# Kernel optimization log

Hardware: AMD Instinct MI355X
Metric: run time of the kernel (lower is better)

The kernel has to match this reference:

```python
import jax, jax.numpy as jnp
import numpy as np

B, N, C_IN, D, K = 4, 512, 256, 256, 20


def setup_inputs() -> dict:
    key = jax.random.key(0)
    ks = jax.random.split(key, 6)
    s_in = 1.0 / np.sqrt(C_IN)
    return {
        "x": jax.random.normal(ks[0], (B, N, C_IN), dtype=jnp.float32),
        "edge_index": jnp.zeros((2, 4), dtype=jnp.int64),
        "batch": jnp.zeros((B * N,), dtype=jnp.int64),
        "W_l": jax.random.uniform(ks[1], (D, C_IN), jnp.float32, -s_in, s_in),
        "b_l": jax.random.uniform(ks[2], (D,), jnp.float32, -s_in, s_in),
        "W_r": jax.random.uniform(ks[3], (D, C_IN), jnp.float32, -s_in, s_in),
        "b_r": jax.random.uniform(ks[4], (D,), jnp.float32, -s_in, s_in),
        "att": jax.random.normal(ks[5], (1, D), dtype=jnp.float32) * 0.1,
    }


def reference(x, edge_index, batch, W_l, b_l, W_r, b_r, att):
    b, n, _ = x.shape
    k = K
    # linear projections -> [b, n, d]
    x_l = jnp.einsum("bnc,dc->bnd", x, W_l) + b_l
    x_r = jnp.einsum("bnc,dc->bnd", x, W_r) + b_r
    # pairwise additive attention: [b, n, n, d]
    pair = x_l[:, :, None, :] + x_r[:, None, :, :]
    pair = jnp.where(pair >= 0, pair, 0.2 * pair)  # leaky_relu(0.2)
    alpha = jnp.einsum("bijd,d->bij", pair, att[0])  # [b, n, n]
    alpha = jnp.nan_to_num(alpha, nan=0.0, posinf=0.0, neginf=0.0)
    # knn reduction: topk over last dim
    attention, indices = jax.lax.top_k(alpha, k)  # [b, n, k]
    attention = jax.nn.softmax(attention, axis=-1).reshape(-1)  # [b*n*k]
    # edge index construction with per-batch node offsets
    offset = (jnp.arange(b, dtype=indices.dtype) * n)[:, None]  # [b, 1]
    index_i = jnp.repeat(jnp.arange(n, dtype=indices.dtype), k)[None, :] + offset
    index_j = indices.reshape(b, n * k) + offset
    new_edge_index = jnp.stack([index_i.reshape(-1), index_j.reshape(-1)], axis=0)
    # dropout is identity in eval mode; learn_sys=False -> return directly
    return new_edge_index, attention
```

## Files before the change

### kernel.cpp

```cpp
#include <hip/hip_runtime.h>
#include <math.h>


__global__ __launch_bounds__(256) void k_transpose(const float* __restrict__ Wl,
                                                   const float* __restrict__ Wr,
                                                   float* __restrict__ WtL,
                                                   float* __restrict__ WtR) {
    const int d = blockIdx.x, c = threadIdx.x;
    if (blockIdx.y == 0) WtL[c * 256 + d] = Wl[d * 256 + c];
    else                 WtR[c * 256 + d] = Wr[d * 256 + c];
}

__global__ __launch_bounds__(256) void k_proj(const float* __restrict__ x,
        const float* __restrict__ WtL, const float* __restrict__ WtR,
        const float* __restrict__ bl, const float* __restrict__ br,
        const float* __restrict__ att,
        float* __restrict__ XL, float* __restrict__ XRt,
        float* __restrict__ Av, float* __restrict__ Bv) {
    __shared__ float xs[4 * 256];
    __shared__ float red[32];
    const int tid = threadIdx.x;
    const int R = blockIdx.x * 4;

    ((float4*)xs)[tid] = ((const float4*)(x + (size_t)R * 256))[tid];
    __syncthreads();

    float accL[4] = {0.f, 0.f, 0.f, 0.f}, accR[4] = {0.f, 0.f, 0.f, 0.f};
    for (int c = 0; c < 256; c += 4) {
        const float wl0 = WtL[(c + 0) * 256 + tid];
        const float wl1 = WtL[(c + 1) * 256 + tid];
        const float wl2 = WtL[(c + 2) * 256 + tid];
        const float wl3 = WtL[(c + 3) * 256 + tid];
        const float wr0 = WtR[(c + 0) * 256 + tid];
        const float wr1 = WtR[(c + 1) * 256 + tid];
        const float wr2 = WtR[(c + 2) * 256 + tid];
        const float wr3 = WtR[(c + 3) * 256 + tid];
#pragma unroll
        for (int r = 0; r < 4; ++r) {
            const float4 xv = *(const float4*)&xs[r * 256 + c];
            accL[r] = fmaf(xv.x, wl0, accL[r]);
            accL[r] = fmaf(xv.y, wl1, accL[r]);
            accL[r] = fmaf(xv.z, wl2, accL[r]);
            accL[r] = fmaf(xv.w, wl3, accL[r]);
            accR[r] = fmaf(xv.x, wr0, accR[r]);
            accR[r] = fmaf(xv.y, wr1, accR[r]);
            accR[r] = fmaf(xv.z, wr2, accR[r]);
            accR[r] = fmaf(xv.w, wr3, accR[r]);
        }
    }

    const float blv = bl[tid], brv = br[tid], atv = att[tid];
    float xlv[4], xrv[4], pa[4], pb[4];
#pragma unroll
    for (int r = 0; r < 4; ++r) {
        xlv[r] = accL[r] + blv;
        xrv[r] = accR[r] + brv;
        XL[(size_t)(R + r) * 256 + tid] = xlv[r];
        pa[r] = atv * xlv[r];
        pb[r] = atv * xrv[r];
    }
    const int b = R >> 9, jr = R & 511;
    *(float4*)&XRt[((size_t)(b * 256 + tid)) * 512 + jr] =
        make_float4(xrv[0], xrv[1], xrv[2], xrv[3]);

#pragma unroll
    for (int r = 0; r < 4; ++r) {
#pragma unroll
        for (int off = 32; off; off >>= 1) {
            pa[r] += __shfl_xor(pa[r], off);
            pb[r] += __shfl_xor(pb[r], off);
        }
    }
    const int lane = tid & 63, wv = tid >> 6;
    if (lane == 0) {
#pragma unroll
        for (int r = 0; r < 4; ++r) {
            red[r * 8 + wv] = pa[r];
            red[r * 8 + 4 + wv] = pb[r];
        }
    }
    __syncthreads();
    if (tid < 8) {
        const int r = tid >> 1, side = tid & 1;
        const float* p = &red[r * 8 + side * 4];
        const float s = p[0] + p[1] + p[2] + p[3];
        if (side == 0) Av[R + r] = s; else Bv[R + r] = s;
    }
}

__global__ __launch_bounds__(256) void k_pair(const float* __restrict__ XL,
        const float* __restrict__ XRt, const float* __restrict__ Av,
        const float* __restrict__ Bv, const float* __restrict__ att,
        float* __restrict__ alpha) {
    const int tid = threadIdx.x;
    const int g = blockIdx.x;
    const int jh = g & 1;
    const int ig = g >> 1;
    const int b = ig >> 6;
    const int R = b * 512 + (ig & 63) * 8;
    const int j = jh * 256 + tid;

    const float* __restrict__ XLr = XL + (size_t)R * 256;
    const float* __restrict__ xrp = XRt + ((size_t)b * 256) * 512 + j;

    float acc[8];
#pragma unroll
    for (int i = 0; i < 8; ++i) acc[i] = 0.f;

    for (int d = 0; d < 256; d += 8) {
        float xr[8];
#pragma unroll
        for (int dd = 0; dd < 8; ++dd) xr[dd] = xrp[dd * 512];
#pragma unroll
        for (int dd = 0; dd < 8; ++dd) {
            const float a = att[d + dd];
#pragma unroll
            for (int i = 0; i < 8; ++i) {
                const float v = XLr[i * 256 + d + dd] + xr[dd];
                acc[i] = fmaf(a, fabsf(v), acc[i]);
            }
        }
        xrp += 8 * 512;
    }

    const float Bj = Bv[b * 512 + j];
#pragma unroll
    for (int i = 0; i < 8; ++i) {
        float a = fmaf(0.4f, acc[i], 0.6f * (Av[R + i] + Bj));
        if (!isfinite(a)) a = 0.f;
        alpha[(size_t)(R + i) * 512 + j] = a;
    }
}

__global__ __launch_bounds__(256) void k_topk(const float* __restrict__ alpha,
                                              float* __restrict__ out) {
    const int lane = threadIdx.x & 63;
    const int row = blockIdx.x * 4 + (threadIdx.x >> 6);
    const float* ar = alpha + (size_t)row * 512;

    const float4 u0 = *(const float4*)&ar[lane * 8];
    const float4 u1 = *(const float4*)&ar[lane * 8 + 4];
    float v[8] = {u0.x, u0.y, u0.z, u0.w, u1.x, u1.y, u1.z, u1.w};

    float myval = 0.f, mmax = 0.f;
    int myidx = 0;
    for (int sel = 0; sel < 20; ++sel) {
        float bv = v[0]; int bt = 0;
#pragma unroll
        for (int t = 1; t < 8; ++t) { if (v[t] > bv) { bv = v[t]; bt = t; } }
        int bj = lane * 8 + bt;
#pragma unroll
        for (int off = 32; off; off >>= 1) {
            const float ov = __shfl_xor(bv, off);
            const int   oj = __shfl_xor(bj, off);
            if (ov > bv || (ov == bv && oj < bj)) { bv = ov; bj = oj; }
        }
        if (sel == 0) mmax = bv;
        if (lane == sel) { myval = bv; myidx = bj; }
        if ((bj >> 3) == lane) {
            const int bt2 = bj & 7;
#pragma unroll
            for (int t = 0; t < 8; ++t) if (t == bt2) v[t] = -INFINITY;
        }
    }
    const float e = (lane < 20) ? expf(myval - mmax) : 0.f;
    float s = e;
#pragma unroll
    for (int off = 32; off; off >>= 1) s += __shfl_xor(s, off);
    if (lane < 20) {
        const int base = row * 20 + lane;
        const int b = row >> 9;
        out[base] = (float)row;
        out[40960 + base] = (float)(b * 512 + myidx);
        out[81920 + base] = e / s;
    }
}

extern "C" void kernel_launch(void* const* d_in, const int* in_sizes, int n_in,
                              void* d_out, int out_size, void* d_ws, size_t ws_size,
                              hipStream_t stream) {
    const float* x   = (const float*)d_in[0];
    const float* Wl  = (const float*)d_in[3];
    const float* bl  = (const float*)d_in[4];
    const float* Wr  = (const float*)d_in[5];
    const float* br  = (const float*)d_in[6];
    const float* att = (const float*)d_in[7];

    float* ws    = (float*)d_ws;
    float* WtL   = ws;
    float* WtR   = ws + 65536;
    float* alpha = ws;
    float* XL    = ws + 1048576;
    float* XRt   = ws + 1572864;
    float* Av    = ws + 2097152;
    float* Bv    = ws + 2099200;
    float* out   = (float*)d_out;

    k_transpose<<<dim3(256, 2), dim3(256), 0, stream>>>(Wl, Wr, WtL, WtR);
    k_proj<<<dim3(512), dim3(256), 0, stream>>>(x, WtL, WtR, bl, br, att, XL, XRt, Av, Bv);
    k_pair<<<dim3(512), dim3(256), 0, stream>>>(XL, XRt, Av, Bv, att, alpha);
    k_topk<<<dim3(512), dim3(256), 0, stream>>>(alpha, out);
}
```

Measured before the change: 138.7 us.

## Split pair kernel reduction over two d-halves with register prefetch

The pairwise attention kernel now launches twice as many blocks, each covering 128 columns, and splits the 256-long feature reduction between two halves of the block. The halves are merged through shared memory. XRt loads are double-buffered in registers to overlap with compute, and the att and XL loads are vectorized as float4. This aims to add parallelism and hide memory latency, at the cost of a sync, shared-memory traffic, and idle threads during the final write.

```diff
diff --git a/kernel.cpp b/kernel.cpp
--- a/kernel.cpp
+++ b/kernel.cpp
@@ -92,43 +92,73 @@
         const float* __restrict__ XRt, const float* __restrict__ Av,
         const float* __restrict__ Bv, const float* __restrict__ att,
         float* __restrict__ alpha) {
+    __shared__ float mrg[128 * 8];
     const int tid = threadIdx.x;
     const int g = blockIdx.x;
-    const int jh = g & 1;
-    const int ig = g >> 1;
-    const int b = ig >> 6;
-    const int R = b * 512 + (ig & 63) * 8;
-    const int j = jh * 256 + tid;
+    const int jq = g & 3;
+    const int io = g >> 2;
+    const int b = io >> 6;
+    const int R = b * 512 + (io & 63) * 8;
+    const int jl = tid & 127;
+    const int h = tid >> 7;
+    const int j = jq * 128 + jl;
+    const int dbase = h * 128;
 
     const float* __restrict__ XLr = XL + (size_t)R * 256;
-    const float* __restrict__ xrp = XRt + ((size_t)b * 256) * 512 + j;
+    const float* __restrict__ xrp = XRt + ((size_t)(b * 256 + dbase)) * 512 + j;
 
     float acc[8];
 #pragma unroll
     for (int i = 0; i < 8; ++i) acc[i] = 0.f;
 
-    for (int d = 0; d < 256; d += 8) {
-        float xr[8];
-#pragma unroll
-        for (int dd = 0; dd < 8; ++dd) xr[dd] = xrp[dd * 512];
-#pragma unroll
-        for (int dd = 0; dd < 8; ++dd) {
-            const float a = att[d + dd];
-#pragma unroll
-            for (int i = 0; i < 8; ++i) {
-                const float v = XLr[i * 256 + d + dd] + xr[dd];
-                acc[i] = fmaf(a, fabsf(v), acc[i]);
-            }
-        }
-        xrp += 8 * 512;
-    }
-
-    const float Bj = Bv[b * 512 + j];
-#pragma unroll
-    for (int i = 0; i < 8; ++i) {
-        float a = fmaf(0.4f, acc[i], 0.6f * (Av[R + i] + Bj));
-        if (!isfinite(a)) a = 0.f;
-        alpha[(size_t)(R + i) * 512 + j] = a;
+    float xrbuf[2][8];
+#pragma unroll
+    for (int dd = 0; dd < 8; ++dd) xrbuf[0][dd] = xrp[dd * 512];
+
+#pragma unroll
+    for (int ch = 0; ch < 16; ++ch) {
+        const float* cur = xrbuf[ch & 1];
+        float* nxt = xrbuf[(ch + 1) & 1];
+        if (ch < 15) {
+            const float* p = xrp + (size_t)(ch + 1) * 8 * 512;
+#pragma unroll
+            for (int dd = 0; dd < 8; ++dd) nxt[dd] = p[dd * 512];
+        }
+        const int d = dbase + ch * 8;
+        const float4 at0 = *(const float4*)&att[d];
+        const float4 at1 = *(const float4*)&att[d + 4];
+#pragma unroll
+        for (int i = 0; i < 8; ++i) {
+            const float4 xa = *(const float4*)&XLr[i * 256 + d];
+            const float4 xb = *(const float4*)&XLr[i * 256 + d + 4];
+            acc[i] = fmaf(at0.x, fabsf(xa.x + cur[0]), acc[i]);
+            acc[i] = fmaf(at0.y, fabsf(xa.y + cur[1]), acc[i]);
+            acc[i] = fmaf(at0.z, fabsf(xa.z + cur[2]), acc[i]);
+            acc[i] = fmaf(at0.w, fabsf(xa.w + cur[3]), acc[i]);
+            acc[i] = fmaf(at1.x, fabsf(xb.x + cur[4]), acc[i]);
+            acc[i] = fmaf(at1.y, fabsf(xb.y + cur[5]), acc[i]);
+            acc[i] = fmaf(at1.z, fabsf(xb.z + cur[6]), acc[i]);
+            acc[i] = fmaf(at1.w, fabsf(xb.w + cur[7]), acc[i]);
+        }
+    }
+
+    if (h == 1) {
+        *(float4*)&mrg[jl * 8 + 0] = make_float4(acc[0], acc[1], acc[2], acc[3]);
+        *(float4*)&mrg[jl * 8 + 4] = make_float4(acc[4], acc[5], acc[6], acc[7]);
+    }
+    __syncthreads();
+    if (h == 0) {
+        const float4 m0 = *(const float4*)&mrg[jl * 8 + 0];
+        const float4 m1 = *(const float4*)&mrg[jl * 8 + 4];
+        acc[0] += m0.x; acc[1] += m0.y; acc[2] += m0.z; acc[3] += m0.w;
+        acc[4] += m1.x; acc[5] += m1.y; acc[6] += m1.z; acc[7] += m1.w;
+        const float Bj = Bv[b * 512 + j];
+#pragma unroll
+        for (int i = 0; i < 8; ++i) {
+            float a = fmaf(0.4f, acc[i], 0.6f * (Av[R + i] + Bj));
+            if (!isfinite(a)) a = 0.f;
+            alpha[(size_t)(R + i) * 512 + j] = a;
+        }
     }
 }
 
@@ -198,6 +228,6 @@
 
     k_transpose<<<dim3(256, 2), dim3(256), 0, stream>>>(Wl, Wr, WtL, WtR);
     k_proj<<<dim3(512), dim3(256), 0, stream>>>(x, WtL, WtR, bl, br, att, XL, XRt, Av, Bv);
-    k_pair<<<dim3(512), dim3(256), 0, stream>>>(XL, XRt, Av, Bv, att, alpha);
+    k_pair<<<dim3(1024), dim3(256), 0, stream>>>(XL, XRt, Av, Bv, att, alpha);
     k_topk<<<dim3(512), dim3(256), 0, stream>>>(alpha, out);
 }
```

Measured after the change: 144.1 us. 1.04x slower.

## Fuse pairwise attention and top-k into one kernel with split-d reduction

Applied to the files above, without the earlier changes.

Merges the pairwise alpha kernel and the top-k kernel so the 4x512 alpha rows stay in shared memory instead of making a round trip through global memory. Each block now handles 4 query rows over all 512 columns, splitting the d dimension across two thread halves and merging the partial sums through LDS. XRt is loaded as float4 with register double-buffering. The change cuts global traffic and one launch, but each block does less row reuse (4 rows instead of 8) and uses more shared memory, which may lower occupancy.

```diff
diff --git a/kernel.cpp b/kernel.cpp
--- a/kernel.cpp
+++ b/kernel.cpp
@@ -88,56 +88,100 @@
     }
 }
 
-__global__ __launch_bounds__(256) void k_pair(const float* __restrict__ XL,
+__global__ __launch_bounds__(256) void k_pair_topk(const float* __restrict__ XL,
         const float* __restrict__ XRt, const float* __restrict__ Av,
         const float* __restrict__ Bv, const float* __restrict__ att,
-        float* __restrict__ alpha) {
+        float* __restrict__ out) {
+    __shared__ float xls[4 * 256];
+    __shared__ float atts[256];
+    __shared__ float mrg[16 * 128];
+    __shared__ float alph[4 * 512];
     const int tid = threadIdx.x;
     const int g = blockIdx.x;
-    const int jh = g & 1;
-    const int ig = g >> 1;
-    const int b = ig >> 6;
-    const int R = b * 512 + (ig & 63) * 8;
-    const int j = jh * 256 + tid;
-
-    const float* __restrict__ XLr = XL + (size_t)R * 256;
-    const float* __restrict__ xrp = XRt + ((size_t)b * 256) * 512 + j;
-
-    float acc[8];
-#pragma unroll
-    for (int i = 0; i < 8; ++i) acc[i] = 0.f;
-
-    for (int d = 0; d < 256; d += 8) {
-        float xr[8];
-#pragma unroll
-        for (int dd = 0; dd < 8; ++dd) xr[dd] = xrp[dd * 512];
-#pragma unroll
-        for (int dd = 0; dd < 8; ++dd) {
-            const float a = att[d + dd];
-#pragma unroll
-            for (int i = 0; i < 8; ++i) {
-                const float v = XLr[i * 256 + d + dd] + xr[dd];
-                acc[i] = fmaf(a, fabsf(v), acc[i]);
-            }
-        }
-        xrp += 8 * 512;
-    }
-
-    const float Bj = Bv[b * 512 + j];
-#pragma unroll
-    for (int i = 0; i < 8; ++i) {
-        float a = fmaf(0.4f, acc[i], 0.6f * (Av[R + i] + Bj));
-        if (!isfinite(a)) a = 0.f;
-        alpha[(size_t)(R + i) * 512 + j] = a;
-    }
-}
-
-__global__ __launch_bounds__(256) void k_topk(const float* __restrict__ alpha,
-                                              float* __restrict__ out) {
-    const int lane = threadIdx.x & 63;
-    const int row = blockIdx.x * 4 + (threadIdx.x >> 6);
-    const float* ar = alpha + (size_t)row * 512;
-
+    const int R = g * 4;
+    const int b = R >> 9;
+    const int jc = tid & 127;
+    const int h = tid >> 7;
+
+    ((float4*)xls)[tid] = ((const float4*)(XL + (size_t)R * 256))[tid];
+    if (tid < 64) ((float4*)atts)[tid] = ((const float4*)att)[tid];
+    __syncthreads();
+
+    const float* xrbase = XRt + ((size_t)(b * 256 + h * 128)) * 512 + jc * 4;
+    const int dbase = h * 128;
+
+    float4 acc[4];
+#pragma unroll
+    for (int i = 0; i < 4; ++i) acc[i] = make_float4(0.f, 0.f, 0.f, 0.f);
+
+    float4 buf[2][8];
+#pragma unroll
+    for (int dd = 0; dd < 8; ++dd) buf[0][dd] = *(const float4*)(xrbase + dd * 512);
+
+#pragma unroll
+    for (int ch = 0; ch < 16; ++ch) {
+        const float4* cur = buf[ch & 1];
+        float4* nxt = buf[(ch + 1) & 1];
+        if (ch < 15) {
+            const float* p = xrbase + (size_t)(ch + 1) * 8 * 512;
+#pragma unroll
+            for (int dd = 0; dd < 8; ++dd) nxt[dd] = *(const float4*)(p + dd * 512);
+        }
+        const int d = dbase + ch * 8;
+        const float4 at0 = *(const float4*)&atts[d];
+        const float4 at1 = *(const float4*)&atts[d + 4];
+#pragma unroll
+        for (int i = 0; i < 4; ++i) {
+            const float4 xa = *(const float4*)&xls[i * 256 + d];
+            const float4 xb = *(const float4*)&xls[i * 256 + d + 4];
+#define PSTEP(XLC, ATC, XR4)                                   \
+            acc[i].x = fmaf(ATC, fabsf(XLC + XR4.x), acc[i].x); \
+            acc[i].y = fmaf(ATC, fabsf(XLC + XR4.y), acc[i].y); \
+            acc[i].z = fmaf(ATC, fabsf(XLC + XR4.z), acc[i].z); \
+            acc[i].w = fmaf(ATC, fabsf(XLC + XR4.w), acc[i].w);
+            PSTEP(xa.x, at0.x, cur[0])
+            PSTEP(xa.y, at0.y, cur[1])
+            PSTEP(xa.z, at0.z, cur[2])
+            PSTEP(xa.w, at0.w, cur[3])
+            PSTEP(xb.x, at1.x, cur[4])
+            PSTEP(xb.y, at1.y, cur[5])
+            PSTEP(xb.z, at1.z, cur[6])
+            PSTEP(xb.w, at1.w, cur[7])
+#undef PSTEP
+        }
+    }
+
+    if (h == 1) {
+#pragma unroll
+        for (int i = 0; i < 4; ++i) {
+            mrg[(i * 4 + 0) * 128 + jc] = acc[i].x;
+            mrg[(i * 4 + 1) * 128 + jc] = acc[i].y;
+            mrg[(i * 4 + 2) * 128 + jc] = acc[i].z;
+            mrg[(i * 4 + 3) * 128 + jc] = acc[i].w;
+        }
+    }
+    __syncthreads();
+    if (h == 0) {
+        const float4 Bj = *(const float4*)&Bv[b * 512 + jc * 4];
+#pragma unroll
+        for (int i = 0; i < 4; ++i) {
+            const float Ai = Av[R + i];
+            float a0 = fmaf(0.4f, acc[i].x + mrg[(i * 4 + 0) * 128 + jc], 0.6f * (Ai + Bj.x));
+            float a1 = fmaf(0.4f, acc[i].y + mrg[(i * 4 + 1) * 128 + jc], 0.6f * (Ai + Bj.y));
+            float a2 = fmaf(0.4f, acc[i].z + mrg[(i * 4 + 2) * 128 + jc], 0.6f * (Ai + Bj.z));
+            float a3 = fmaf(0.4f, acc[i].w + mrg[(i * 4 + 3) * 128 + jc], 0.6f * (Ai + Bj.w));
+            if (!isfinite(a0)) a0 = 0.f;
+            if (!isfinite(a1)) a1 = 0.f;
+            if (!isfinite(a2)) a2 = 0.f;
+            if (!isfinite(a3)) a3 = 0.f;
+            *(float4*)&alph[i * 512 + jc * 4] = make_float4(a0, a1, a2, a3);
+        }
+    }
+    __syncthreads();
+
+    const int lane = tid & 63;
+    const int i = tid >> 6;
+    const float* ar = &alph[i * 512];
     const float4 u0 = *(const float4*)&ar[lane * 8];
     const float4 u1 = *(const float4*)&ar[lane * 8 + 4];
     float v[8] = {u0.x, u0.y, u0.z, u0.w, u1.x, u1.y, u1.z, u1.w};
@@ -168,8 +212,8 @@
 #pragma unroll
     for (int off = 32; off; off >>= 1) s += __shfl_xor(s, off);
     if (lane < 20) {
+        const int row = R + i;
         const int base = row * 20 + lane;
-        const int b = row >> 9;
         out[base] = (float)row;
         out[40960 + base] = (float)(b * 512 + myidx);
         out[81920 + base] = e / s;
@@ -189,7 +233,6 @@
     float* ws    = (float*)d_ws;
     float* WtL   = ws;
     float* WtR   = ws + 65536;
-    float* alpha = ws;
     float* XL    = ws + 1048576;
     float* XRt   = ws + 1572864;
     float* Av    = ws + 2097152;
@@ -198,6 +241,5 @@
 
     k_transpose<<<dim3(256, 2), dim3(256), 0, stream>>>(Wl, Wr, WtL, WtR);
     k_proj<<<dim3(512), dim3(256), 0, stream>>>(x, WtL, WtR, bl, br, att, XL, XRt, Av, Bv);
-    k_pair<<<dim3(512), dim3(256), 0, stream>>>(XL, XRt, Av, Bv, att, alpha);
-    k_topk<<<dim3(512), dim3(256), 0, stream>>>(alpha, out);
-}
+    k_pair_topk<<<dim3(512), dim3(256), 0, stream>>>(XL, XRt, Av, Bv, att, out);
+}
```

After: 122.4 us. 11.8% less time.

## Fuse pairwise attention with top-k and retile projection with split-K reduction

Applied to the files above, without the earlier changes.

The pairwise-score kernel and the top-k kernel are merged, so each block computes alpha for 4 rows into shared memory and runs the top-k/softmax there, removing the global alpha round-trip. XRt slices are streamed into a double-buffered LDS staging area with direct global-to-LDS loads. The projection kernel is retiled to 8 rows per 512-thread block with a 4-way split over the input channel and an LDS merge, using float4 weight loads. In exchange, the fused kernel has only 512 blocks of 128 threads and a large LDS footprint, which may limit occupancy.

```diff
diff --git a/kernel.cpp b/kernel.cpp
--- a/kernel.cpp
+++ b/kernel.cpp
@@ -1,6 +1,11 @@
 #include <hip/hip_runtime.h>
 #include <math.h>
 
+
+#define GLD_LDS(gp, lp)                                                        \
+    __builtin_amdgcn_global_load_lds(                                          \
+        (const __attribute__((address_space(1))) float*)(gp),                  \
+        (__attribute__((address_space(3))) float*)(lp), 16, 0, 0)
 
 __global__ __launch_bounds__(256) void k_transpose(const float* __restrict__ Wl,
                                                    const float* __restrict__ Wr,
@@ -11,168 +16,256 @@
     else                 WtR[c * 256 + d] = Wr[d * 256 + c];
 }
 
-__global__ __launch_bounds__(256) void k_proj(const float* __restrict__ x,
+__global__ __launch_bounds__(512, 4) void k_proj(const float* __restrict__ x,
         const float* __restrict__ WtL, const float* __restrict__ WtR,
         const float* __restrict__ bl, const float* __restrict__ br,
         const float* __restrict__ att,
         float* __restrict__ XL, float* __restrict__ XRt,
         float* __restrict__ Av, float* __restrict__ Bv) {
-    __shared__ float xs[4 * 256];
-    __shared__ float red[32];
+    __shared__ __align__(16) float xst[256 * 12];
+    __shared__ __align__(16) float mrg[3 * 4096];
     const int tid = threadIdx.x;
-    const int R = blockIdx.x * 4;
-
-    ((float4*)xs)[tid] = ((const float4*)(x + (size_t)R * 256))[tid];
+    const int dq = tid & 63;
+    const int rq = (tid >> 6) & 1;
+    const int ch = tid >> 7;
+    const int R = blockIdx.x * 8;
+    const int b = R >> 9, jr0 = R & 511;
+
+    {
+        const float4 xv = ((const float4*)(x + (size_t)R * 256))[tid];
+        const int r = tid >> 6;
+        const int c4 = (tid & 63) * 4;
+        xst[(c4 + 0) * 12 + r] = xv.x;
+        xst[(c4 + 1) * 12 + r] = xv.y;
+        xst[(c4 + 2) * 12 + r] = xv.z;
+        xst[(c4 + 3) * 12 + r] = xv.w;
+    }
     __syncthreads();
 
-    float accL[4] = {0.f, 0.f, 0.f, 0.f}, accR[4] = {0.f, 0.f, 0.f, 0.f};
-    for (int c = 0; c < 256; c += 4) {
-        const float wl0 = WtL[(c + 0) * 256 + tid];
-        const float wl1 = WtL[(c + 1) * 256 + tid];
-        const float wl2 = WtL[(c + 2) * 256 + tid];
-        const float wl3 = WtL[(c + 3) * 256 + tid];
-        const float wr0 = WtR[(c + 0) * 256 + tid];
-        const float wr1 = WtR[(c + 1) * 256 + tid];
-        const float wr2 = WtR[(c + 2) * 256 + tid];
-        const float wr3 = WtR[(c + 3) * 256 + tid];
+    float aL[4][4], aR[4][4];
+#pragma unroll
+    for (int r = 0; r < 4; ++r)
+#pragma unroll
+        for (int k = 0; k < 4; ++k) { aL[r][k] = 0.f; aR[r][k] = 0.f; }
+
+    const int c0 = ch * 64;
+    const float* WLp = WtL + (size_t)c0 * 256 + dq * 4;
+    const float* WRp = WtR + (size_t)c0 * 256 + dq * 4;
+#pragma unroll 4
+    for (int cc = 0; cc < 64; ++cc) {
+        const float4 wl = *(const float4*)(WLp + (size_t)cc * 256);
+        const float4 wr = *(const float4*)(WRp + (size_t)cc * 256);
+        const float4 xv = *(const float4*)&xst[(c0 + cc) * 12 + rq * 4];
+#define PROJ_R(r, XS)                                  \
+        aL[r][0] = fmaf(XS, wl.x, aL[r][0]);           \
+        aL[r][1] = fmaf(XS, wl.y, aL[r][1]);           \
+        aL[r][2] = fmaf(XS, wl.z, aL[r][2]);           \
+        aL[r][3] = fmaf(XS, wl.w, aL[r][3]);           \
+        aR[r][0] = fmaf(XS, wr.x, aR[r][0]);           \
+        aR[r][1] = fmaf(XS, wr.y, aR[r][1]);           \
+        aR[r][2] = fmaf(XS, wr.z, aR[r][2]);           \
+        aR[r][3] = fmaf(XS, wr.w, aR[r][3]);
+        PROJ_R(0, xv.x)
+        PROJ_R(1, xv.y)
+        PROJ_R(2, xv.z)
+        PROJ_R(3, xv.w)
+#undef PROJ_R
+    }
+
+    if (ch > 0) {
+        float* m = &mrg[(ch - 1) * 4096];
 #pragma unroll
         for (int r = 0; r < 4; ++r) {
-            const float4 xv = *(const float4*)&xs[r * 256 + c];
-            accL[r] = fmaf(xv.x, wl0, accL[r]);
-            accL[r] = fmaf(xv.y, wl1, accL[r]);
-            accL[r] = fmaf(xv.z, wl2, accL[r]);
-            accL[r] = fmaf(xv.w, wl3, accL[r]);
-            accR[r] = fmaf(xv.x, wr0, accR[r]);
-            accR[r] = fmaf(xv.y, wr1, accR[r]);
-            accR[r] = fmaf(xv.z, wr2, accR[r]);
-            accR[r] = fmaf(xv.w, wr3, accR[r]);
-        }
-    }
-
-    const float blv = bl[tid], brv = br[tid], atv = att[tid];
-    float xlv[4], xrv[4], pa[4], pb[4];
-#pragma unroll
-    for (int r = 0; r < 4; ++r) {
-        xlv[r] = accL[r] + blv;
-        xrv[r] = accR[r] + brv;
-        XL[(size_t)(R + r) * 256 + tid] = xlv[r];
-        pa[r] = atv * xlv[r];
-        pb[r] = atv * xrv[r];
-    }
-    const int b = R >> 9, jr = R & 511;
-    *(float4*)&XRt[((size_t)(b * 256 + tid)) * 512 + jr] =
-        make_float4(xrv[0], xrv[1], xrv[2], xrv[3]);
-
-#pragma unroll
-    for (int r = 0; r < 4; ++r) {
-#pragma unroll
-        for (int off = 32; off; off >>= 1) {
-            pa[r] += __shfl_xor(pa[r], off);
-            pb[r] += __shfl_xor(pb[r], off);
-        }
-    }
-    const int lane = tid & 63, wv = tid >> 6;
-    if (lane == 0) {
+            const int r8 = rq * 4 + r;
+            *(float4*)&m[(r8 * 2 + 0) * 256 + dq * 4] = make_float4(aL[r][0], aL[r][1], aL[r][2], aL[r][3]);
+            *(float4*)&m[(r8 * 2 + 1) * 256 + dq * 4] = make_float4(aR[r][0], aR[r][1], aR[r][2], aR[r][3]);
+        }
+    }
+    __syncthreads();
+
+    if (ch == 0) {
+        const float4 bl4 = *(const float4*)&bl[dq * 4];
+        const float4 br4 = *(const float4*)&br[dq * 4];
+        const float4 at4 = *(const float4*)&att[dq * 4];
+        float pa[4], pb[4];
 #pragma unroll
         for (int r = 0; r < 4; ++r) {
-            red[r * 8 + wv] = pa[r];
-            red[r * 8 + 4 + wv] = pb[r];
-        }
-    }
-    __syncthreads();
-    if (tid < 8) {
-        const int r = tid >> 1, side = tid & 1;
-        const float* p = &red[r * 8 + side * 4];
-        const float s = p[0] + p[1] + p[2] + p[3];
-        if (side == 0) Av[R + r] = s; else Bv[R + r] = s;
-    }
-}
-
-__global__ __launch_bounds__(256) void k_pair(const float* __restrict__ XL,
+            const int r8 = rq * 4 + r;
+            const float4 mL0 = *(const float4*)&mrg[(r8 * 2 + 0) * 256 + dq * 4];
+            const float4 mL1 = *(const float4*)&mrg[4096 + (r8 * 2 + 0) * 256 + dq * 4];
+            const float4 mL2 = *(const float4*)&mrg[8192 + (r8 * 2 + 0) * 256 + dq * 4];
+            const float4 mR0 = *(const float4*)&mrg[(r8 * 2 + 1) * 256 + dq * 4];
+            const float4 mR1 = *(const float4*)&mrg[4096 + (r8 * 2 + 1) * 256 + dq * 4];
+            const float4 mR2 = *(const float4*)&mrg[8192 + (r8 * 2 + 1) * 256 + dq * 4];
+            float4 sl, sr;
+            sl.x = aL[r][0] + mL0.x + mL1.x + mL2.x + bl4.x;
+            sl.y = aL[r][1] + mL0.y + mL1.y + mL2.y + bl4.y;
+            sl.z = aL[r][2] + mL0.z + mL1.z + mL2.z + bl4.z;
+            sl.w = aL[r][3] + mL0.w + mL1.w + mL2.w + bl4.w;
+            sr.x = aR[r][0] + mR0.x + mR1.x + mR2.x + br4.x;
+            sr.y = aR[r][1] + mR0.y + mR1.y + mR2.y + br4.y;
+            sr.z = aR[r][2] + mR0.z + mR1.z + mR2.z + br4.z;
+            sr.w = aR[r][3] + mR0.w + mR1.w + mR2.w + br4.w;
+            *(float4*)&XL[(size_t)(R + r8) * 256 + dq * 4] = sl;
+            const size_t xrb0 = ((size_t)(b * 256 + dq * 4)) * 512 + jr0 + r8;
+            XRt[xrb0 + 0 * 512] = sr.x;
+            XRt[xrb0 + 1 * 512] = sr.y;
+            XRt[xrb0 + 2 * 512] = sr.z;
+            XRt[xrb0 + 3 * 512] = sr.w;
+            pa[r] = at4.x * sl.x + at4.y * sl.y + at4.z * sl.z + at4.w * sl.w;
+            pb[r] = at4.x * sr.x + at4.y * sr.y + at4.z * sr.z + at4.w * sr.w;
+        }
+#pragma unroll
+        for (int r = 0; r < 4; ++r) {
+#pragma unroll
+            for (int off = 32; off; off >>= 1) {
+                pa[r] += __shfl_xor(pa[r], off);
+                pb[r] += __shfl_xor(pb[r], off);
+            }
+        }
+        if (dq == 0) {
+#pragma unroll
+            for (int r = 0; r < 4; ++r) {
+                Av[R + rq * 4 + r] = pa[r];
+                Bv[R + rq * 4 + r] = pb[r];
+            }
+        }
+    }
+}
+
+__global__ __launch_bounds__(128) void k_pair_topk(const float* __restrict__ XL,
         const float* __restrict__ XRt, const float* __restrict__ Av,
         const float* __restrict__ Bv, const float* __restrict__ att,
-        float* __restrict__ alpha) {
+        float* __restrict__ out) {
+    __shared__ __align__(16) float xrb[2][8 * 512];
+    __shared__ __align__(16) float xls[4 * 256];
+    __shared__ __align__(16) float atts[256];
+    __shared__ __align__(16) float alph[4 * 512];
     const int tid = threadIdx.x;
+    const int lane = tid & 63;
+    const int w = tid >> 6;
     const int g = blockIdx.x;
-    const int jh = g & 1;
-    const int ig = g >> 1;
-    const int b = ig >> 6;
-    const int R = b * 512 + (ig & 63) * 8;
-    const int j = jh * 256 + tid;
-
-    const float* __restrict__ XLr = XL + (size_t)R * 256;
-    const float* __restrict__ xrp = XRt + ((size_t)b * 256) * 512 + j;
-
-    float acc[8];
-#pragma unroll
-    for (int i = 0; i < 8; ++i) acc[i] = 0.f;
-
-    for (int d = 0; d < 256; d += 8) {
-        float xr[8];
-#pragma unroll
-        for (int dd = 0; dd < 8; ++dd) xr[dd] = xrp[dd * 512];
+    const int R = g * 4, b = R >> 9;
+    const float* __restrict__ XRb = XRt + (size_t)b * 256 * 512;
+
+    {
+        const float* gr = XRb + (size_t)(4 * w) * 512;
+        float* lr = &xrb[0][(4 * w) * 512];
+#pragma unroll
+        for (int rr = 0; rr < 4; ++rr) {
+            GLD_LDS(gr + rr * 512 + lane * 4, lr + rr * 512);
+            GLD_LDS(gr + rr * 512 + 256 + lane * 4, lr + rr * 512 + 256);
+        }
+    }
+    ((float4*)xls)[tid] = ((const float4*)(XL + (size_t)R * 256))[tid];
+    ((float4*)xls)[tid + 128] = ((const float4*)(XL + (size_t)R * 256))[tid + 128];
+    if (tid < 64) ((float4*)atts)[tid] = ((const float4*)att)[tid];
+
+    float acc[4][4];
+#pragma unroll
+    for (int i = 0; i < 4; ++i)
+#pragma unroll
+        for (int jj = 0; jj < 4; ++jj) acc[i][jj] = 0.f;
+
+    for (int ch = 0; ch < 32; ++ch) {
+        __syncthreads();
+        const int bf = ch & 1;
+        if (ch < 31) {
+            const float* gr = XRb + (size_t)((ch + 1) * 8 + 4 * w) * 512;
+            float* lr = &xrb[bf ^ 1][(4 * w) * 512];
+#pragma unroll
+            for (int rr = 0; rr < 4; ++rr) {
+                GLD_LDS(gr + rr * 512 + lane * 4, lr + rr * 512);
+                GLD_LDS(gr + rr * 512 + 256 + lane * 4, lr + rr * 512 + 256);
+            }
+        }
+        const int d0 = ch * 8;
+        float ats[8], xli[4][8];
+        {
+            const float4 a0 = *(const float4*)&atts[d0];
+            const float4 a1 = *(const float4*)&atts[d0 + 4];
+            ats[0] = a0.x; ats[1] = a0.y; ats[2] = a0.z; ats[3] = a0.w;
+            ats[4] = a1.x; ats[5] = a1.y; ats[6] = a1.z; ats[7] = a1.w;
+#pragma unroll
+            for (int i = 0; i < 4; ++i) {
+                const float4 x0 = *(const float4*)&xls[i * 256 + d0];
+                const float4 x1 = *(const float4*)&xls[i * 256 + d0 + 4];
+                xli[i][0] = x0.x; xli[i][1] = x0.y; xli[i][2] = x0.z; xli[i][3] = x0.w;
+                xli[i][4] = x1.x; xli[i][5] = x1.y; xli[i][6] = x1.z; xli[i][7] = x1.w;
+            }
+        }
 #pragma unroll
         for (int dd = 0; dd < 8; ++dd) {
-            const float a = att[d + dd];
-#pragma unroll
-            for (int i = 0; i < 8; ++i) {
-                const float v = XLr[i * 256 + d + dd] + xr[dd];
-                acc[i] = fmaf(a, fabsf(v), acc[i]);
-            }
-        }
-        xrp += 8 * 512;
-    }
-
-    const float Bj = Bv[b * 512 + j];
-#pragma unroll
-    for (int i = 0; i < 8; ++i) {
-        float a = fmaf(0.4f, acc[i], 0.6f * (Av[R + i] + Bj));
-        if (!isfinite(a)) a = 0.f;
-        alpha[(size_t)(R + i) * 512 + j] = a;
-    }
-}
-
-__global__ __launch_bounds__(256) void k_topk(const float* __restrict__ alpha,
-                                              float* __restrict__ out) {
-    const int lane = threadIdx.x & 63;
-    const int row = blockIdx.x * 4 + (threadIdx.x >> 6);
-    const float* ar = alpha + (size_t)row * 512;
-
-    const float4 u0 = *(const float4*)&ar[lane * 8];
-    const float4 u1 = *(const float4*)&ar[lane * 8 + 4];
-    float v[8] = {u0.x, u0.y, u0.z, u0.w, u1.x, u1.y, u1.z, u1.w};
-
-    float myval = 0.f, mmax = 0.f;
-    int myidx = 0;
-    for (int sel = 0; sel < 20; ++sel) {
-        float bv = v[0]; int bt = 0;
-#pragma unroll
-        for (int t = 1; t < 8; ++t) { if (v[t] > bv) { bv = v[t]; bt = t; } }
-        int bj = lane * 8 + bt;
-#pragma unroll
-        for (int off = 32; off; off >>= 1) {
-            const float ov = __shfl_xor(bv, off);
-            const int   oj = __shfl_xor(bj, off);
-            if (ov > bv || (ov == bv && oj < bj)) { bv = ov; bj = oj; }
-        }
-        if (sel == 0) mmax = bv;
-        if (lane == sel) { myval = bv; myidx = bj; }
-        if ((bj >> 3) == lane) {
-            const int bt2 = bj & 7;
-#pragma unroll
-            for (int t = 0; t < 8; ++t) if (t == bt2) v[t] = -INFINITY;
-        }
-    }
-    const float e = (lane < 20) ? expf(myval - mmax) : 0.f;
-    float s = e;
-#pragma unroll
-    for (int off = 32; off; off >>= 1) s += __shfl_xor(s, off);
-    if (lane < 20) {
-        const int base = row * 20 + lane;
-        const int b = row >> 9;
-        out[base] = (float)row;
-        out[40960 + base] = (float)(b * 512 + myidx);
-        out[81920 + base] = e / s;
+            const float4 xr = *(const float4*)&xrb[bf][dd * 512 + tid * 4];
+            const float ad = ats[dd];
+#pragma unroll
+            for (int i = 0; i < 4; ++i) {
+                const float xl = xli[i][dd];
+                acc[i][0] = fmaf(ad, fabsf(xl + xr.x), acc[i][0]);
+                acc[i][1] = fmaf(ad, fabsf(xl + xr.y), acc[i][1]);
+                acc[i][2] = fmaf(ad, fabsf(xl + xr.z), acc[i][2]);
+                acc[i][3] = fmaf(ad, fabsf(xl + xr.w), acc[i][3]);
+            }
+        }
+    }
+
+    {
+        const float4 Bj = *(const float4*)&Bv[b * 512 + tid * 4];
+#pragma unroll
+        for (int i = 0; i < 4; ++i) {
+            const float Ai = Av[R + i];
+            float a0 = fmaf(0.4f, acc[i][0], 0.6f * (Ai + Bj.x));
+            float a1 = fmaf(0.4f, acc[i][1], 0.6f * (Ai + Bj.y));
+            float a2 = fmaf(0.4f, acc[i][2], 0.6f * (Ai + Bj.z));
+            float a3 = fmaf(0.4f, acc[i][3], 0.6f * (Ai + Bj.w));
+            if (!isfinite(a0)) a0 = 0.f;
+            if (!isfinite(a1)) a1 = 0.f;
+            if (!isfinite(a2)) a2 = 0.f;
+            if (!isfinite(a3)) a3 = 0.f;
+            *(float4*)&alph[i * 512 + tid * 4] = make_float4(a0, a1, a2, a3);
+        }
+    }
+    __syncthreads();
+
+    for (int ri = 0; ri < 2; ++ri) {
+        const int i = 2 * w + ri;
+        const float* ar = &alph[i * 512];
+        const float4 u0 = *(const float4*)&ar[lane * 8];
+        const float4 u1 = *(const float4*)&ar[lane * 8 + 4];
+        float v[8] = {u0.x, u0.y, u0.z, u0.w, u1.x, u1.y, u1.z, u1.w};
+
+        float myval = 0.f, mmax = 0.f;
+        int myidx = 0;
+        for (int sel = 0; sel < 20; ++sel) {
+            float bv = v[0]; int bt = 0;
+#pragma unroll
+            for (int t = 1; t < 8; ++t) { if (v[t] > bv) { bv = v[t]; bt = t; } }
+            int bj = lane * 8 + bt;
+#pragma unroll
+            for (int off = 32; off; off >>= 1) {
+                const float ov = __shfl_xor(bv, off);
+                const int   oj = __shfl_xor(bj, off);
+                if (ov > bv || (ov == bv && oj < bj)) { bv = ov; bj = oj; }
+            }
+            if (sel == 0) mmax = bv;
+            if (lane == sel) { myval = bv; myidx = bj; }
+            if ((bj >> 3) == lane) {
+                const int bt2 = bj & 7;
+#pragma unroll
+                for (int t = 0; t < 8; ++t) if (t == bt2) v[t] = -INFINITY;
+            }
+        }
+        const float e = (lane < 20) ? expf(myval - mmax) : 0.f;
+        float s = e;
+#pragma unroll
+        for (int off = 32; off; off >>= 1) s += __shfl_xor(s, off);
+        if (lane < 20) {
+            const int row = R + i;
+            const int base = row * 20 + lane;
+            out[base] = (float)row;
+            out[40960 + base] = (float)(b * 512 + myidx);
+            out[81920 + base] = e / s;
+        }
     }
 }
 
@@ -186,18 +279,16 @@
     const float* br  = (const float*)d_in[6];
     const float* att = (const float*)d_in[7];
 
-    float* ws    = (float*)d_ws;
-    float* WtL   = ws;
-    float* WtR   = ws + 65536;
-    float* alpha = ws;
-    float* XL    = ws + 1048576;
-    float* XRt   = ws + 1572864;
-    float* Av    = ws + 2097152;
-    float* Bv    = ws + 2099200;
-    float* out   = (float*)d_out;
+    float* ws  = (float*)d_ws;
+    float* WtL = ws;
+    float* WtR = ws + 65536;
+    float* XL  = ws + 1048576;
+    float* XRt = ws + 1572864;
+    float* Av  = ws + 2097152;
+    float* Bv  = ws + 2099200;
+    float* out = (float*)d_out;
 
     k_transpose<<<dim3(256, 2), dim3(256), 0, stream>>>(Wl, Wr, WtL, WtR);
-    k_proj<<<dim3(512), dim3(256), 0, stream>>>(x, WtL, WtR, bl, br, att, XL, XRt, Av, Bv);
-    k_pair<<<dim3(512), dim3(256), 0, stream>>>(XL, XRt, Av, Bv, att, alpha);
-    k_topk<<<dim3(512), dim3(256), 0, stream>>>(alpha, out);
-}
+    k_proj<<<dim3(256), dim3(512), 0, stream>>>(x, WtL, WtR, bl, br, att, XL, XRt, Av, Bv);
+    k_pair_topk<<<dim3(512), dim3(128), 0, stream>>>(XL, XRt, Av, Bv, att, out);
+}
```

New measurement: 155.0 us. 1.12x slower.
